# Kernel optimization log

Measured on AMD Instinct MI355X. Metric: run time of the kernel, lower is better.

The kernel has to match this reference:

```python
import jax, jax.numpy as jnp
import numpy as np
import math

N_EMB = 768
N_HEAD = 12
N_INNER = 3072
B, T = 2, 2048
EPS = 1e-4


def _gelu_tanh(x):
    return x * 0.5 * (1.0 + jnp.tanh(math.sqrt(2.0 / math.pi) * (x + 0.044715 * x ** 3)))


def _layernorm(x, scale, bias):
    mean = jnp.mean(x, axis=-1, keepdims=True)
    var = jnp.var(x, axis=-1, keepdims=True, ddof=1)  # torch.var default: unbiased
    return scale * ((x - mean) / jnp.sqrt(var + EPS)) + bias


def setup_inputs() -> dict:
    key = jax.random.key(0)
    ks = jax.random.split(key, 16)
    s_attn = 1.0 / math.sqrt(N_EMB)
    s_mlp1 = 1.0 / math.sqrt(N_EMB)
    s_mlp2 = 1.0 / math.sqrt(N_INNER)
    return {
        "x": jax.random.normal(ks[0], (B, T, N_EMB), dtype=jnp.float32),
        "Wq": jax.random.normal(ks[1], (N_EMB, N_EMB), dtype=jnp.float32) * s_attn,
        "bq": jnp.zeros((N_EMB,), jnp.float32),
        "Wk": jax.random.normal(ks[2], (N_EMB, N_EMB), dtype=jnp.float32) * s_attn,
        "bk": jnp.zeros((N_EMB,), jnp.float32),
        "Wv": jax.random.normal(ks[3], (N_EMB, N_EMB), dtype=jnp.float32) * s_attn,
        "bv": jnp.zeros((N_EMB,), jnp.float32),
        "Wo": jax.random.normal(ks[4], (N_EMB, N_EMB), dtype=jnp.float32) * s_attn,
        "bo": jnp.zeros((N_EMB,), jnp.float32),
        "ln1_s": jnp.ones((N_EMB,), jnp.float32),
        "ln1_b": jnp.zeros((N_EMB,), jnp.float32),
        "W1": jax.random.normal(ks[5], (N_EMB, N_INNER), dtype=jnp.float32) * s_mlp1,
        "b1": jnp.zeros((N_INNER,), jnp.float32),
        "W2": jax.random.normal(ks[6], (N_INNER, N_EMB), dtype=jnp.float32) * s_mlp2,
        "b2": jnp.zeros((N_EMB,), jnp.float32),
        "ln2_s": jnp.ones((N_EMB,), jnp.float32),
        "ln2_b": jnp.zeros((N_EMB,), jnp.float32),
    }


def reference(x, Wq, bq, Wk, bk, Wv, bv, Wo, bo, ln1_s, ln1_b, W1, b1, W2, b2, ln2_s, ln2_b):
    Bx, Tx, C = x.shape
    dh = C // N_HEAD
    # QKV projections -> [B, H, T, dh]
    def split_heads(y):
        return y.reshape(Bx, Tx, N_HEAD, dh).transpose(0, 2, 1, 3)
    q = split_heads(x @ Wq + bq)
    k = split_heads(x @ Wk + bk)
    v = split_heads(x @ Wv + bv)
    # naive full-score causal attention (materializes [B,H,T,T])
    scores = jnp.einsum("bhqd,bhkd->bhqk", q, k)
    causal = jnp.tril(jnp.ones((Tx, Tx), dtype=bool))
    scores = jnp.where(causal, scores, -jnp.inf)
    attn = jax.nn.softmax(scores / math.sqrt(dh), axis=-1)
    ctx = jnp.einsum("bhqk,bhkd->bhqd", attn, v)
    ctx = ctx.transpose(0, 2, 1, 3).reshape(Bx, Tx, C)
    attn_out = ctx @ Wo + bo
    # post-norm residual
    h = _layernorm(x + attn_out, ln1_s, ln1_b)
    mlp_out = _gelu_tanh(h @ W1 + b1) @ W2 + b2
    return _layernorm(h + mlp_out, ln2_s, ln2_b)
```

## Files before the change

kernel.cpp:

```cpp
#include <hip/hip_runtime.h>
#include <math.h>

#define TB  2
#define TT  2048
#define TC  768
#define TH  12
#define TDH 64
#define TI  3072
#define TM  (TB*TT)

typedef __attribute__((ext_vector_type(8))) __bf16 bf16x8;
typedef __attribute__((ext_vector_type(4))) __bf16 bf16x4;
typedef __attribute__((ext_vector_type(4))) float  f32x4;

__device__ __forceinline__ float gelu_tanh(float x) {
    float x3 = x * x * x;
    return 0.5f * x * (1.0f + tanhf(0.7978845608028654f * (x + 0.044715f * x3)));
}

__device__ __forceinline__ void gld_lds16(const void* g, void* l) {
    __builtin_amdgcn_global_load_lds(
        (const __attribute__((address_space(1))) unsigned int*)g,
        (__attribute__((address_space(3))) unsigned int*)l,
        16, 0, 0);
}

template<int N>
__device__ __forceinline__ void vmcnt_wait() {
    if constexpr (N == 0)      asm volatile("s_waitcnt vmcnt(0)" ::: "memory");
    else if constexpr (N == 2) asm volatile("s_waitcnt vmcnt(2)" ::: "memory");
    else if constexpr (N == 3) asm volatile("s_waitcnt vmcnt(3)" ::: "memory");
    else if constexpr (N == 4) asm volatile("s_waitcnt vmcnt(4)" ::: "memory");
    else if constexpr (N == 6) asm volatile("s_waitcnt vmcnt(6)" ::: "memory");
    else if constexpr (N == 8) asm volatile("s_waitcnt vmcnt(8)" ::: "memory");
    else static_assert(N == 0, "unsupported vmcnt");
}

#define BK 32

template<int BM_, int BN_, int WM_, int WN_, int THREADS_>
__global__ __launch_bounds__(THREADS_)
void gemm_mfma(const __bf16* __restrict__ A, const __bf16* __restrict__ Bt,
               const float* __restrict__ b0, const float* __restrict__ b1,
               const float* __restrict__ b2, const float* __restrict__ resid,
               float* __restrict__ outf, __bf16* __restrict__ outb,
               int N, int K, size_t wt_stride, size_t out_stride, int ep)
{
    constexpr int WAVES_N = BN_ / WN_;
    constexpr int TMt = WM_ / 16, TNt = WN_ / 16;
    constexpr int RP   = THREADS_ / 4;
    constexpr int AISS = BM_ / RP, BISS = BN_ / RP;
    constexpr int S    = AISS + BISS;
    constexpr int PASS = THREADS_ * 16;
    constexpr int TILE = (BM_ + BN_) * BK;
    static_assert(AISS >= 1 && BISS >= 1, "tile too small for thread count");
    __shared__ __align__(16) __bf16 lds[3 * TILE];

    const int tid  = threadIdx.x;
    const int wave = tid >> 6, lane = tid & 63;
    const int wm = wave / WAVES_N, wn = wave % WAVES_N;
    const int m0 = blockIdx.y * BM_, n0 = blockIdx.x * BN_;
    const int z  = blockIdx.z;

    const __bf16* Bz = Bt + (size_t)z * wt_stride;
    const size_t Kb = (size_t)K * 2;
    const char* Ag = (const char*)A + (size_t)m0 * Kb;
    const char* Bg = (const char*)Bz + (size_t)n0 * Kb;
    const int srow = tid >> 2;
    const int scol = ((tid & 3) ^ ((tid >> 4) & 3)) * 16;
    const int wbase = wave * 1024;

    f32x4 acc[TMt][TNt];
    #pragma unroll
    for (int i = 0; i < TMt; ++i)
        #pragma unroll
        for (int j = 0; j < TNt; ++j)
            acc[i][j] = (f32x4){0.f, 0.f, 0.f, 0.f};

    const int arow = wm * WM_ + (lane & 15);
    const int brow = wn * WN_ + (lane & 15);
    const int koff = (((lane >> 4) ^ ((lane >> 2) & 3))) * 8;

    const int nIter = K / BK;

    auto stage = [&](char* base, int k0b) {
        #pragma unroll
        for (int s = 0; s < AISS; ++s)
            gld_lds16(Ag + (size_t)(srow + RP * s) * Kb + k0b + scol,
                      base + s * PASS + wbase);
        char* bbase = base + BM_ * BK * 2;
        #pragma unroll
        for (int s = 0; s < BISS; ++s)
            gld_lds16(Bg + (size_t)(srow + RP * s) * Kb + k0b + scol,
                      bbase + s * PASS + wbase);
    };

    char* P0 = (char*)lds;
    char* P1 = P0 + (size_t)TILE * 2;
    char* P2 = P1 + (size_t)TILE * 2;

    stage(P0, 0);
    if (nIter > 1) stage(P1, BK * 2);
    __builtin_amdgcn_sched_barrier(0);
    char* cur = P0; char* n1 = P1; char* n2 = P2;

    for (int it = 0; it < nIter; ++it) {
        if (it + 2 < nIter) stage(n2, (it + 2) * (BK * 2));
        __builtin_amdgcn_sched_barrier(0);
        const int rem = nIter - 1 - it;
        if (rem >= 2)      vmcnt_wait<2 * S>();
        else if (rem == 1) vmcnt_wait<S>();
        else               vmcnt_wait<0>();
        __builtin_amdgcn_s_barrier();
        __builtin_amdgcn_sched_barrier(0);

        const __bf16* As = (const __bf16*)cur;
        const __bf16* Bs = As + BM_ * BK;
        bf16x8 af[TMt], bfr[TNt];
        #pragma unroll
        for (int ti = 0; ti < TMt; ++ti)
            af[ti] = *(const bf16x8*)&As[(arow + ti * 16) * BK + koff];
        #pragma unroll
        for (int tj = 0; tj < TNt; ++tj)
            bfr[tj] = *(const bf16x8*)&Bs[(brow + tj * 16) * BK + koff];
        #pragma unroll
        for (int ti = 0; ti < TMt; ++ti)
            #pragma unroll
            for (int tj = 0; tj < TNt; ++tj)
                acc[ti][tj] = __builtin_amdgcn_mfma_f32_16x16x32_bf16(
                    af[ti], bfr[tj], acc[ti][tj], 0, 0, 0);

        __builtin_amdgcn_sched_barrier(0);
        __builtin_amdgcn_s_barrier();
        char* t = cur; cur = n1; n1 = n2; n2 = t;
    }

    const int lrow = m0 + wm * WM_ + ((lane >> 4) << 2);
    const int lcol = n0 + wn * WN_ + (lane & 15);

    if (ep == 0) {
        const float* bias = (z == 0) ? b0 : (z == 1) ? b1 : b2;
        __bf16* outz = outb + (size_t)z * out_stride;
        if (z < 2) {
            #pragma unroll
            for (int tj = 0; tj < TNt; ++tj) {
                int n = lcol + tj * 16;
                float bj = bias[n];
                int h = n >> 6, d = n & 63;
                #pragma unroll
                for (int ti = 0; ti < TMt; ++ti)
                    #pragma unroll
                    for (int r = 0; r < 4; ++r) {
                        int m = lrow + ti * 16 + r;
                        int b = m >> 11, t = m & (TT - 1);
                        outz[((size_t)(b * TH + h) * TT + t) * TDH + d] =
                            (__bf16)(acc[ti][tj][r] + bj);
                    }
            }
        } else {
            #pragma unroll
            for (int tj = 0; tj < TNt; ++tj) {
                int n = lcol + tj * 16;
                float bj = bias[n];
                int h = n >> 6, d = n & 63;
                #pragma unroll
                for (int ti = 0; ti < TMt; ++ti) {
                    int m = lrow + ti * 16;
                    int b = m >> 11, t0 = m & (TT - 1);
                    bf16x4 pk;
                    #pragma unroll
                    for (int r = 0; r < 4; ++r)
                        pk[r] = (__bf16)(acc[ti][tj][r] + bj);
                    *(bf16x4*)(outz + ((size_t)(b * TH + h) * TDH + d) * TT + t0) = pk;
                }
            }
        }
    } else if (ep == 1) {
        #pragma unroll
        for (int tj = 0; tj < TNt; ++tj) {
            int n = lcol + tj * 16;
            float bj = b0[n];
            #pragma unroll
            for (int ti = 0; ti < TMt; ++ti)
                #pragma unroll
                for (int r = 0; r < 4; ++r) {
                    int m = lrow + ti * 16 + r;
                    outf[(size_t)m * N + n] =
                        acc[ti][tj][r] + bj + resid[(size_t)m * N + n];
                }
        }
    } else {
        #pragma unroll
        for (int tj = 0; tj < TNt; ++tj) {
            int n = lcol + tj * 16;
            float bj = b0[n];
            #pragma unroll
            for (int ti = 0; ti < TMt; ++ti)
                #pragma unroll
                for (int r = 0; r < 4; ++r) {
                    int m = lrow + ti * 16 + r;
                    outb[(size_t)m * N + n] = (__bf16)gelu_tanh(acc[ti][tj][r] + bj);
                }
        }
    }
}

__global__ __launch_bounds__(256)
void prep_kernel(const float* __restrict__ x,
                 const float* __restrict__ Wq, const float* __restrict__ Wk,
                 const float* __restrict__ Wv, const float* __restrict__ Wo,
                 const float* __restrict__ W1, const float* __restrict__ W2,
                 __bf16* __restrict__ x_bf, __bf16* __restrict__ WqkvT,
                 __bf16* __restrict__ WoT, __bf16* __restrict__ W1T,
                 __bf16* __restrict__ W2T)
{
    const size_t WSZ = (size_t)TC * TC;
    int bid = blockIdx.x;
    if (bid < 1536) {
        int i = (bid * 256 + threadIdx.x) * 8;
        float4 a = *(const float4*)(x + i);
        float4 b = *(const float4*)(x + i + 4);
        bf16x8 v;
        v[0] = (__bf16)a.x; v[1] = (__bf16)a.y; v[2] = (__bf16)a.z; v[3] = (__bf16)a.w;
        v[4] = (__bf16)b.x; v[5] = (__bf16)b.y; v[6] = (__bf16)b.z; v[7] = (__bf16)b.w;
        *(bf16x8*)(x_bf + i) = v;
        return;
    }
    bid -= 1536;
    const float* src; __bf16* dst; int K, N, tloc;
    if (bid < 2304) {
        int w = bid / 576; tloc = bid - w * 576;
        K = TC; N = TC;
        src = (w == 0) ? Wq : (w == 1) ? Wk : (w == 2) ? Wv : Wo;
        dst = (w < 3) ? (WqkvT + (size_t)w * WSZ) : WoT;
    } else if (bid < 4608) {
        tloc = bid - 2304; K = TC; N = TI; src = W1; dst = W1T;
    } else {
        tloc = bid - 4608; K = TI; N = TC; src = W2; dst = W2T;
    }
    int tiles_x = N >> 5;
    int n0 = (tloc % tiles_x) * 32, k0 = (tloc / tiles_x) * 32;

    __shared__ float tile[32][33];
    const int tx = threadIdx.x & 31, ty = threadIdx.x >> 5;
    #pragma unroll
    for (int i = 0; i < 32; i += 8)
        tile[ty + i][tx] = src[(size_t)(k0 + ty + i) * N + n0 + tx];
    __syncthreads();
    #pragma unroll
    for (int i = 0; i < 32; i += 8)
        dst[(size_t)(n0 + ty + i) * K + k0 + tx] = (__bf16)tile[tx][ty + i];
}

__global__ __launch_bounds__(256)
void ln_kernel(const float* __restrict__ in, const float* __restrict__ gs,
               const float* __restrict__ gb, float* __restrict__ out,
               __bf16* __restrict__ out_bf)
{
    const int row = blockIdx.x, tid = threadIdx.x;
    const float* r = in + (size_t)row * TC;
    float x0 = r[tid], x1 = r[tid + 256], x2 = r[tid + 512];
    float s = x0 + x1 + x2;
    float q = x0 * x0 + x1 * x1 + x2 * x2;
    #pragma unroll
    for (int off = 32; off > 0; off >>= 1) {
        s += __shfl_down(s, off);
        q += __shfl_down(q, off);
    }
    __shared__ float partial[8];
    __shared__ float stats[2];
    int wid = tid >> 6, lane = tid & 63;
    if (lane == 0) { partial[wid] = s; partial[wid + 4] = q; }
    __syncthreads();
    if (tid == 0) {
        float S = partial[0] + partial[1] + partial[2] + partial[3];
        float Q = partial[4] + partial[5] + partial[6] + partial[7];
        float mean = S * (1.0f / (float)TC);
        float var = (Q - (float)TC * mean * mean) * (1.0f / (float)(TC - 1));
        stats[0] = mean;
        stats[1] = rsqrtf(var + 1e-4f);
    }
    __syncthreads();
    float mean = stats[0], rstd = stats[1];
    float* w = out + (size_t)row * TC;
    float y0 = gs[tid]       * ((x0 - mean) * rstd) + gb[tid];
    float y1 = gs[tid + 256] * ((x1 - mean) * rstd) + gb[tid + 256];
    float y2 = gs[tid + 512] * ((x2 - mean) * rstd) + gb[tid + 512];
    w[tid] = y0; w[tid + 256] = y1; w[tid + 512] = y2;
    if (out_bf) {
        __bf16* wb = out_bf + (size_t)row * TC;
        wb[tid] = (__bf16)y0; wb[tid + 256] = (__bf16)y1; wb[tid + 512] = (__bf16)y2;
    }
}

#define AP 72
#define VP 136
#define ATT_SCALE 0.18033688011112042f

__global__ __launch_bounds__(256)
void attn_mfma(const __bf16* __restrict__ Q, const __bf16* __restrict__ K,
               const __bf16* __restrict__ Vt, __bf16* __restrict__ ctx)
{
    __shared__ __align__(16) __bf16 Ks[128 * AP];
    __shared__ __align__(16) __bf16 Vs[64 * VP];
    __shared__ __align__(16) __bf16 Ps[64 * VP];

    const int tid  = threadIdx.x;
    const int wave = tid >> 6, lane = tid & 63;
    const int c = lane & 15, g = lane >> 4;
    const int bh = blockIdx.y;
    const int qi = blockIdx.x;
    const int qt = (qi & 1) ? (31 - (qi >> 1)) : (qi >> 1);
    const int q_glob = qt * 64 + wave * 16 + c;

    const __bf16* Qb = Q  + (size_t)bh * TT * TDH;
    const __bf16* Kb = K  + (size_t)bh * TT * TDH;
    const __bf16* Vb = Vt + (size_t)bh * TDH * TT;

    bf16x8 qf0 = *(const bf16x8*)(Qb + (size_t)q_glob * TDH + g * 8);
    bf16x8 qf1 = *(const bf16x8*)(Qb + (size_t)q_glob * TDH + 32 + g * 8);

    const int krow = tid >> 3, kcol = (tid & 7) * 8;
    const int vrow = tid >> 4, vcol = (tid & 15) * 8;

    float m_i = -1e30f, l_i = 0.0f;
    f32x4 acc[4];
    #pragma unroll
    for (int m2 = 0; m2 < 4; ++m2) acc[m2] = (f32x4){0.f, 0.f, 0.f, 0.f};

    const int pmax = qt >> 1;
    for (int p = 0; p <= pmax; ++p) {
        const int kb = p * 128;
        bf16x8 kv[4], vv[4];
        #pragma unroll
        for (int s = 0; s < 4; ++s) {
            kv[s] = *(const bf16x8*)(Kb + (size_t)(kb + krow + 32 * s) * TDH + kcol);
            vv[s] = *(const bf16x8*)(Vb + (size_t)(vrow + 16 * s) * TT + kb + vcol);
        }
        __syncthreads();
        #pragma unroll
        for (int s = 0; s < 4; ++s) {
            *(bf16x8*)&Ks[(krow + 32 * s) * AP + kcol] = kv[s];
            *(bf16x8*)&Vs[(vrow + 16 * s) * VP + vcol] = vv[s];
        }
        __syncthreads();

        f32x4 st[8];
        #pragma unroll
        for (int g2 = 0; g2 < 8; ++g2) {
            bf16x8 af0 = *(const bf16x8*)&Ks[(16 * g2 + c) * AP + g * 8];
            bf16x8 af1 = *(const bf16x8*)&Ks[(16 * g2 + c) * AP + 32 + g * 8];
            f32x4 z = (f32x4){0.f, 0.f, 0.f, 0.f};
            z = __builtin_amdgcn_mfma_f32_16x16x32_bf16(af0, qf0, z, 0, 0, 0);
            z = __builtin_amdgcn_mfma_f32_16x16x32_bf16(af1, qf1, z, 0, 0, 0);
            st[g2] = z;
        }

        float sv[8][4];
        float mx = -1e30f;
        if (p == pmax) {
            #pragma unroll
            for (int g2 = 0; g2 < 8; ++g2)
                #pragma unroll
                for (int r = 0; r < 4; ++r) {
                    int kcol2 = kb + 16 * g2 + 4 * g + r;
                    float v = (kcol2 > q_glob) ? -1e30f : st[g2][r] * ATT_SCALE;
                    sv[g2][r] = v;
                    mx = fmaxf(mx, v);
                }
        } else {
            #pragma unroll
            for (int g2 = 0; g2 < 8; ++g2)
                #pragma unroll
                for (int r = 0; r < 4; ++r) {
                    float v = st[g2][r] * ATT_SCALE;
                    sv[g2][r] = v;
                    mx = fmaxf(mx, v);
                }
        }
        mx = fmaxf(mx, __shfl_xor(mx, 16));
        mx = fmaxf(mx, __shfl_xor(mx, 32));

        float nm = m_i;
        if (!__all(mx <= m_i + 8.0f)) {
            nm = fmaxf(m_i, mx);
            float corr = exp2f(m_i - nm);
            l_i *= corr;
            #pragma unroll
            for (int m2 = 0; m2 < 4; ++m2) {
                acc[m2][0] *= corr; acc[m2][1] *= corr;
                acc[m2][2] *= corr; acc[m2][3] *= corr;
            }
            m_i = nm;
        }

        float ps = 0.f;
        #pragma unroll
        for (int g2 = 0; g2 < 8; ++g2) {
            bf16x4 pk;
            #pragma unroll
            for (int r = 0; r < 4; ++r) {
                float pp = exp2f(sv[g2][r] - nm);
                ps += pp;
                pk[r] = (__bf16)pp;
            }
            *(bf16x4*)&Ps[(wave * 16 + c) * VP + 16 * g2 + 4 * g] = pk;
        }
        ps += __shfl_xor(ps, 16);
        ps += __shfl_xor(ps, 32);
        l_i += ps;

        bf16x8 pf[4];
        #pragma unroll
        for (int s = 0; s < 4; ++s)
            pf[s] = *(const bf16x8*)&Ps[(wave * 16 + c) * VP + 32 * s + g * 8];
        #pragma unroll
        for (int m2 = 0; m2 < 4; ++m2) {
            #pragma unroll
            for (int s = 0; s < 4; ++s) {
                bf16x8 vf = *(const bf16x8*)&Vs[(16 * m2 + c) * VP + 32 * s + g * 8];
                acc[m2] = __builtin_amdgcn_mfma_f32_16x16x32_bf16(vf, pf[s], acc[m2], 0, 0, 0);
            }
        }
    }

    const int b = bh / TH, h = bh - b * TH;
    float inv = 1.0f / l_i;
    #pragma unroll
    for (int m2 = 0; m2 < 4; ++m2) {
        bf16x4 o;
        #pragma unroll
        for (int r = 0; r < 4; ++r)
            o[r] = (__bf16)(acc[m2][r] * inv);
        *(bf16x4*)(ctx + ((size_t)b * TT + q_glob) * TC + h * TDH + 16 * m2 + 4 * g) = o;
    }
}

extern "C" void kernel_launch(void* const* d_in, const int* in_sizes, int n_in,
                              void* d_out, int out_size, void* d_ws, size_t ws_size,
                              hipStream_t stream)
{
    const float* x    = (const float*)d_in[0];
    const float* Wq   = (const float*)d_in[1];
    const float* bq   = (const float*)d_in[2];
    const float* Wk   = (const float*)d_in[3];
    const float* bk   = (const float*)d_in[4];
    const float* Wv   = (const float*)d_in[5];
    const float* bv   = (const float*)d_in[6];
    const float* Wo   = (const float*)d_in[7];
    const float* bo   = (const float*)d_in[8];
    const float* ln1s = (const float*)d_in[9];
    const float* ln1b = (const float*)d_in[10];
    const float* W1   = (const float*)d_in[11];
    const float* b1   = (const float*)d_in[12];
    const float* W2   = (const float*)d_in[13];
    const float* b2   = (const float*)d_in[14];
    const float* ln2s = (const float*)d_in[15];
    const float* ln2b = (const float*)d_in[16];
    float* out = (float*)d_out;

    const size_t MC  = (size_t)TM * TC;
    const size_t MCB = MC * 2;
    const size_t WSZ = (size_t)TC * TC;
    const size_t W12 = (size_t)TC * TI;

    char* W = (char*)d_ws;
    __bf16* qkvb  = (__bf16*)W;
    __bf16* x_bf  = (__bf16*)(W + 3 * MCB);
    float*  tmp1  = (float*)W;
    __bf16* u_bf  = (__bf16*)W;
    float*  h_f32 = (float*)(W + 4 * MCB);
    __bf16* ctxh  = (__bf16*)(W + 6 * MCB);
    __bf16* wts   = (__bf16*)(W + 7 * MCB);
    __bf16* WqkvT = wts;
    __bf16* WoT   = WqkvT + 3 * WSZ;
    __bf16* W1T   = WoT + WSZ;
    __bf16* W2T   = W1T + W12;

    prep_kernel<<<dim3(1536 + 6912), dim3(256), 0, stream>>>(
        x, Wq, Wk, Wv, Wo, W1, W2, x_bf, WqkvT, WoT, W1T, W2T);

    gemm_mfma<128, 128, 64, 32, 512><<<dim3(TC / 128, TM / 128, 3), dim3(512), 0, stream>>>(
        x_bf, WqkvT, bq, bk, bv, nullptr, nullptr, qkvb, TC, TC, WSZ, MC, 0);

    attn_mfma<<<dim3(TT / 64, TB * TH), dim3(256), 0, stream>>>(
        qkvb, qkvb + MC, qkvb + 2 * MC, ctxh);

    gemm_mfma<64, 64, 32, 32, 256><<<dim3(TC / 64, TM / 64, 1), dim3(256), 0, stream>>>(
        ctxh, WoT, bo, nullptr, nullptr, x, tmp1, nullptr, TC, TC, 0, 0, 1);

    ln_kernel<<<dim3(TM), dim3(256), 0, stream>>>(tmp1, ln1s, ln1b, h_f32, ctxh);

    gemm_mfma<128, 128, 64, 32, 512><<<dim3(TI / 128, TM / 128, 1), dim3(512), 0, stream>>>(
        ctxh, W1T, b1, nullptr, nullptr, nullptr, nullptr, u_bf, TI, TC, 0, 0, 2);

    gemm_mfma<64, 64, 32, 32, 256><<<dim3(TC / 64, TM / 64, 1), dim3(256), 0, stream>>>(
        u_bf, W2T, b2, nullptr, nullptr, h_f32, out, nullptr, TC, TI, 0, 0, 1);

    ln_kernel<<<dim3(TM), dim3(256), 0, stream>>>(out, ln2s, ln2b, out, nullptr);
}
```

Measured before the change: 312.0 us.

## Restructure attention to 32x32 MFMA with split-KV waves and swizzled LDS

The attention kernel now uses 32x32x16 bf16 MFMA instead of 16x16x32. Each pair of waves shares 32 query rows and the two pairs split each 128-key block into two 64-key halves, then merge their softmax states through LDS at the end. The K and V shared tiles drop their padding and use an XOR swizzle to avoid bank conflicts, and each wave gets a private P buffer. The aim is fewer LDS fragment reads and fewer shuffle reductions per tile, in exchange for an extra merge pass and higher register pressure from the 16-wide accumulators.

```diff
diff --git a/kernel.cpp b/kernel.cpp
--- a/kernel.cpp
+++ b/kernel.cpp
@@ -9,9 +9,10 @@
 #define TI  3072
 #define TM  (TB*TT)
 
-typedef __attribute__((ext_vector_type(8))) __bf16 bf16x8;
-typedef __attribute__((ext_vector_type(4))) __bf16 bf16x4;
-typedef __attribute__((ext_vector_type(4))) float  f32x4;
+typedef __attribute__((ext_vector_type(8)))  __bf16 bf16x8;
+typedef __attribute__((ext_vector_type(4)))  __bf16 bf16x4;
+typedef __attribute__((ext_vector_type(4)))  float  f32x4;
+typedef __attribute__((ext_vector_type(16))) float  f32x16;
 
 __device__ __forceinline__ float gelu_tanh(float x) {
     float x3 = x * x * x;
@@ -293,40 +294,48 @@
     }
 }
 
-#define AP 72
-#define VP 136
+#define PP 72
 #define ATT_SCALE 0.18033688011112042f
 
 __global__ __launch_bounds__(256)
 void attn_mfma(const __bf16* __restrict__ Q, const __bf16* __restrict__ K,
                const __bf16* __restrict__ Vt, __bf16* __restrict__ ctx)
 {
-    __shared__ __align__(16) __bf16 Ks[128 * AP];
-    __shared__ __align__(16) __bf16 Vs[64 * VP];
-    __shared__ __align__(16) __bf16 Ps[64 * VP];
+    __shared__ __align__(16) __bf16 Ks[128 * 64];
+    __shared__ __align__(16) __bf16 Vs[64 * 128];
+    __shared__ __align__(16) __bf16 Ps[4 * 32 * PP];
 
     const int tid  = threadIdx.x;
     const int wave = tid >> 6, lane = tid & 63;
-    const int c = lane & 15, g = lane >> 4;
+    const int l31 = lane & 31, h5 = lane >> 5, l7 = lane & 7;
+    const int q32  = wave & 1;
+    const int wgrp = wave >> 1;
     const int bh = blockIdx.y;
     const int qi = blockIdx.x;
     const int qt = (qi & 1) ? (31 - (qi >> 1)) : (qi >> 1);
-    const int q_glob = qt * 64 + wave * 16 + c;
+    const int q_glob = qt * 64 + q32 * 32 + l31;
 
     const __bf16* Qb = Q  + (size_t)bh * TT * TDH;
     const __bf16* Kb = K  + (size_t)bh * TT * TDH;
     const __bf16* Vb = Vt + (size_t)bh * TDH * TT;
 
-    bf16x8 qf0 = *(const bf16x8*)(Qb + (size_t)q_glob * TDH + g * 8);
-    bf16x8 qf1 = *(const bf16x8*)(Qb + (size_t)q_glob * TDH + 32 + g * 8);
-
-    const int krow = tid >> 3, kcol = (tid & 7) * 8;
-    const int vrow = tid >> 4, vcol = (tid & 15) * 8;
+    bf16x8 qf[4];
+    #pragma unroll
+    for (int ks = 0; ks < 4; ++ks)
+        qf[ks] = *(const bf16x8*)(Qb + (size_t)q_glob * TDH + ks * 16 + h5 * 8);
+
+    const int krow = tid >> 3;
+    const int kchW = ((tid & 7) ^ (krow & 7)) * 8;
+    const int vrow = tid >> 4;
+    const int vch  = tid & 15;
+    const int vchW = (((vch & 7) ^ (vrow & 7)) | (vch & 8)) * 8;
 
     float m_i = -1e30f, l_i = 0.0f;
-    f32x4 acc[4];
-    #pragma unroll
-    for (int m2 = 0; m2 < 4; ++m2) acc[m2] = (f32x4){0.f, 0.f, 0.f, 0.f};
+    f32x16 acc[2];
+    acc[0] = (f32x16)(0.0f);
+    acc[1] = (f32x16)(0.0f);
+
+    __bf16* PsW = Ps + wave * 32 * PP;
 
     const int pmax = qt >> 1;
     for (int p = 0; p <= pmax; ++p) {
@@ -334,105 +343,135 @@
         bf16x8 kv[4], vv[4];
         #pragma unroll
         for (int s = 0; s < 4; ++s) {
-            kv[s] = *(const bf16x8*)(Kb + (size_t)(kb + krow + 32 * s) * TDH + kcol);
-            vv[s] = *(const bf16x8*)(Vb + (size_t)(vrow + 16 * s) * TT + kb + vcol);
+            kv[s] = *(const bf16x8*)(Kb + (size_t)(kb + krow + 32 * s) * TDH + (tid & 7) * 8);
+            vv[s] = *(const bf16x8*)(Vb + (size_t)(vrow + 16 * s) * TT + kb + vch * 8);
         }
         __syncthreads();
         #pragma unroll
         for (int s = 0; s < 4; ++s) {
-            *(bf16x8*)&Ks[(krow + 32 * s) * AP + kcol] = kv[s];
-            *(bf16x8*)&Vs[(vrow + 16 * s) * VP + vcol] = vv[s];
+            *(bf16x8*)&Ks[(krow + 32 * s) * 64 + kchW]  = kv[s];
+            *(bf16x8*)&Vs[(vrow + 16 * s) * 128 + vchW] = vv[s];
         }
         __syncthreads();
 
-        f32x4 st[8];
-        #pragma unroll
-        for (int g2 = 0; g2 < 8; ++g2) {
-            bf16x8 af0 = *(const bf16x8*)&Ks[(16 * g2 + c) * AP + g * 8];
-            bf16x8 af1 = *(const bf16x8*)&Ks[(16 * g2 + c) * AP + 32 + g * 8];
-            f32x4 z = (f32x4){0.f, 0.f, 0.f, 0.f};
-            z = __builtin_amdgcn_mfma_f32_16x16x32_bf16(af0, qf0, z, 0, 0, 0);
-            z = __builtin_amdgcn_mfma_f32_16x16x32_bf16(af1, qf1, z, 0, 0, 0);
-            st[g2] = z;
-        }
-
-        float sv[8][4];
+        f32x16 st[2];
+        #pragma unroll
+        for (int t = 0; t < 2; ++t) {
+            const int rowk = wgrp * 64 + 32 * t + l31;
+            f32x16 z = (f32x16)(0.0f);
+            #pragma unroll
+            for (int ks = 0; ks < 4; ++ks) {
+                const int ch = ((ks * 2 + h5) ^ (l7)) * 8;
+                bf16x8 af = *(const bf16x8*)&Ks[rowk * 64 + ch];
+                z = __builtin_amdgcn_mfma_f32_32x32x16_bf16(af, qf[ks], z, 0, 0, 0);
+            }
+            st[t] = z;
+        }
+
         float mx = -1e30f;
         if (p == pmax) {
             #pragma unroll
-            for (int g2 = 0; g2 < 8; ++g2)
-                #pragma unroll
-                for (int r = 0; r < 4; ++r) {
-                    int kcol2 = kb + 16 * g2 + 4 * g + r;
-                    float v = (kcol2 > q_glob) ? -1e30f : st[g2][r] * ATT_SCALE;
-                    sv[g2][r] = v;
+            for (int t = 0; t < 2; ++t)
+                #pragma unroll
+                for (int r = 0; r < 16; ++r) {
+                    int kvg = kb + wgrp * 64 + 32 * t + (r & 3) + 8 * (r >> 2) + 4 * h5;
+                    float v = (kvg > q_glob) ? -1e30f : st[t][r] * ATT_SCALE;
+                    st[t][r] = v;
                     mx = fmaxf(mx, v);
                 }
         } else {
             #pragma unroll
-            for (int g2 = 0; g2 < 8; ++g2)
-                #pragma unroll
-                for (int r = 0; r < 4; ++r) {
-                    float v = st[g2][r] * ATT_SCALE;
-                    sv[g2][r] = v;
+            for (int t = 0; t < 2; ++t)
+                #pragma unroll
+                for (int r = 0; r < 16; ++r) {
+                    float v = st[t][r] * ATT_SCALE;
+                    st[t][r] = v;
                     mx = fmaxf(mx, v);
                 }
         }
-        mx = fmaxf(mx, __shfl_xor(mx, 16));
         mx = fmaxf(mx, __shfl_xor(mx, 32));
 
-        float nm = m_i;
         if (!__all(mx <= m_i + 8.0f)) {
-            nm = fmaxf(m_i, mx);
+            float nm = fmaxf(m_i, mx);
             float corr = exp2f(m_i - nm);
             l_i *= corr;
-            #pragma unroll
-            for (int m2 = 0; m2 < 4; ++m2) {
-                acc[m2][0] *= corr; acc[m2][1] *= corr;
-                acc[m2][2] *= corr; acc[m2][3] *= corr;
+            acc[0] *= corr;
+            acc[1] *= corr;
+            m_i = nm;
+        }
+
+        float ps = 0.f;
+        #pragma unroll
+        for (int t = 0; t < 2; ++t)
+            #pragma unroll
+            for (int a = 0; a < 4; ++a) {
+                bf16x4 pk;
+                #pragma unroll
+                for (int i = 0; i < 4; ++i) {
+                    float pp = exp2f(st[t][4 * a + i] - m_i);
+                    ps += pp;
+                    pk[i] = (__bf16)pp;
+                }
+                *(bf16x4*)&PsW[l31 * PP + 32 * t + 8 * a + 4 * h5] = pk;
             }
-            m_i = nm;
-        }
-
-        float ps = 0.f;
-        #pragma unroll
-        for (int g2 = 0; g2 < 8; ++g2) {
-            bf16x4 pk;
-            #pragma unroll
-            for (int r = 0; r < 4; ++r) {
-                float pp = exp2f(sv[g2][r] - nm);
-                ps += pp;
-                pk[r] = (__bf16)pp;
-            }
-            *(bf16x4*)&Ps[(wave * 16 + c) * VP + 16 * g2 + 4 * g] = pk;
-        }
-        ps += __shfl_xor(ps, 16);
         ps += __shfl_xor(ps, 32);
         l_i += ps;
 
         bf16x8 pf[4];
         #pragma unroll
-        for (int s = 0; s < 4; ++s)
-            pf[s] = *(const bf16x8*)&Ps[(wave * 16 + c) * VP + 32 * s + g * 8];
-        #pragma unroll
-        for (int m2 = 0; m2 < 4; ++m2) {
-            #pragma unroll
-            for (int s = 0; s < 4; ++s) {
-                bf16x8 vf = *(const bf16x8*)&Vs[(16 * m2 + c) * VP + 32 * s + g * 8];
-                acc[m2] = __builtin_amdgcn_mfma_f32_16x16x32_bf16(vf, pf[s], acc[m2], 0, 0, 0);
+        for (int ks = 0; ks < 4; ++ks)
+            pf[ks] = *(const bf16x8*)&PsW[l31 * PP + ks * 16 + h5 * 8];
+        #pragma unroll
+        for (int m2 = 0; m2 < 2; ++m2) {
+            const int d = m2 * 32 + l31;
+            #pragma unroll
+            for (int ks = 0; ks < 4; ++ks) {
+                const int ch = (wgrp * 8 + (((ks * 2 + h5) ^ (l7)))) * 8;
+                bf16x8 vf = *(const bf16x8*)&Vs[d * 128 + ch];
+                acc[m2] = __builtin_amdgcn_mfma_f32_32x32x16_bf16(vf, pf[ks], acc[m2], 0, 0, 0);
             }
         }
     }
 
-    const int b = bh / TH, h = bh - b * TH;
-    float inv = 1.0f / l_i;
-    #pragma unroll
-    for (int m2 = 0; m2 < 4; ++m2) {
-        bf16x4 o;
-        #pragma unroll
-        for (int r = 0; r < 4; ++r)
-            o[r] = (__bf16)(acc[m2][r] * inv);
-        *(bf16x4*)(ctx + ((size_t)b * TT + q_glob) * TC + h * TDH + 16 * m2 + 4 * g) = o;
+    __syncthreads();
+    float* accb0 = (float*)Ks;
+    float* accb1 = (float*)Ps;
+    float* mlb   = (float*)Vs;
+    if (wave >= 2) {
+        float* ab = (wave == 2) ? accb0 : accb1;
+        #pragma unroll
+        for (int m2 = 0; m2 < 2; ++m2)
+            #pragma unroll
+            for (int j = 0; j < 16; ++j)
+                ab[lane * 33 + m2 * 16 + j] = acc[m2][j];
+        mlb[(wave - 2) * 128 + lane] = m_i;
+        mlb[(wave - 2) * 128 + 64 + lane] = l_i;
+    }
+    __syncthreads();
+    if (wave < 2) {
+        float* ab = (wave == 0) ? accb0 : accb1;
+        float mo = mlb[wave * 128 + lane];
+        float lo = mlb[wave * 128 + 64 + lane];
+        float nm = fmaxf(m_i, mo);
+        float a = exp2f(m_i - nm), bw = exp2f(mo - nm);
+        float l = a * l_i + bw * lo;
+        float inv = 1.0f / l;
+        const int b = bh / TH, h = bh - b * TH;
+        #pragma unroll
+        for (int m2 = 0; m2 < 2; ++m2) {
+            #pragma unroll
+            for (int ag = 0; ag < 4; ++ag) {
+                bf16x4 o;
+                #pragma unroll
+                for (int i = 0; i < 4; ++i) {
+                    int r = 4 * ag + i;
+                    float v = a * acc[m2][r] + bw * ab[lane * 33 + m2 * 16 + r];
+                    o[i] = (__bf16)(v * inv);
+                }
+                int d0 = m2 * 32 + 8 * ag + 4 * h5;
+                *(bf16x4*)(ctx + ((size_t)b * TT + q_glob) * TC + h * TDH + d0) = o;
+            }
+        }
     }
 }
 
```

Measured after the change: 323.5 us. +3.7%, slower.

## Split-K the W2 GEMM with atomic accumulation onto LN1 output plus bias

Applied to the files above, without the earlier changes.

The down-projection GEMM (K=3072) is split into two K halves along grid z. Each half atomically adds its partial sums into the output buffer. The LN1 kernel pre-initialises that buffer with h + b2, which removes the separate residual read and the h_f32 buffer. This doubles the block count to fill more CUs on a long-K GEMM with few output tiles, at the cost of fp32 atomics on every output element and a non-deterministic summation order.

```diff
diff --git a/kernel.cpp b/kernel.cpp
--- a/kernel.cpp
+++ b/kernel.cpp
@@ -44,7 +44,8 @@
                const float* __restrict__ b0, const float* __restrict__ b1,
                const float* __restrict__ b2, const float* __restrict__ resid,
                float* __restrict__ outf, __bf16* __restrict__ outb,
-               int N, int K, size_t wt_stride, size_t out_stride, int ep)
+               int N, int K, int Krow, size_t wt_stride, size_t a_zoff,
+               size_t out_stride, int ep)
 {
     constexpr int WAVES_N = BN_ / WN_;
     constexpr int TMt = WM_ / 16, TNt = WN_ / 16;
@@ -63,8 +64,8 @@
     const int z  = blockIdx.z;
 
     const __bf16* Bz = Bt + (size_t)z * wt_stride;
-    const size_t Kb = (size_t)K * 2;
-    const char* Ag = (const char*)A + (size_t)m0 * Kb;
+    const size_t Kb = (size_t)Krow * 2;
+    const char* Ag = (const char*)A + (size_t)m0 * Kb + (size_t)z * a_zoff;
     const char* Bg = (const char*)Bz + (size_t)n0 * Kb;
     const int srow = tid >> 2;
     const int scol = ((tid & 3) ^ ((tid >> 4) & 3)) * 16;
@@ -189,7 +190,7 @@
                         acc[ti][tj][r] + bj + resid[(size_t)m * N + n];
                 }
         }
-    } else {
+    } else if (ep == 2) {
         #pragma unroll
         for (int tj = 0; tj < TNt; ++tj) {
             int n = lcol + tj * 16;
@@ -200,6 +201,18 @@
                 for (int r = 0; r < 4; ++r) {
                     int m = lrow + ti * 16 + r;
                     outb[(size_t)m * N + n] = (__bf16)gelu_tanh(acc[ti][tj][r] + bj);
+                }
+        }
+    } else {
+        #pragma unroll
+        for (int tj = 0; tj < TNt; ++tj) {
+            int n = lcol + tj * 16;
+            #pragma unroll
+            for (int ti = 0; ti < TMt; ++ti)
+                #pragma unroll
+                for (int r = 0; r < 4; ++r) {
+                    int m = lrow + ti * 16 + r;
+                    atomicAdd(&outf[(size_t)m * N + n], acc[ti][tj][r]);
                 }
         }
     }
@@ -255,7 +268,8 @@
 __global__ __launch_bounds__(256)
 void ln_kernel(const float* __restrict__ in, const float* __restrict__ gs,
                const float* __restrict__ gb, float* __restrict__ out,
-               __bf16* __restrict__ out_bf)
+               __bf16* __restrict__ out_bf,
+               const float* __restrict__ ib, float* __restrict__ io)
 {
     const int row = blockIdx.x, tid = threadIdx.x;
     const float* r = in + (size_t)row * TC;
@@ -282,14 +296,22 @@
     }
     __syncthreads();
     float mean = stats[0], rstd = stats[1];
-    float* w = out + (size_t)row * TC;
     float y0 = gs[tid]       * ((x0 - mean) * rstd) + gb[tid];
     float y1 = gs[tid + 256] * ((x1 - mean) * rstd) + gb[tid + 256];
     float y2 = gs[tid + 512] * ((x2 - mean) * rstd) + gb[tid + 512];
-    w[tid] = y0; w[tid + 256] = y1; w[tid + 512] = y2;
+    if (out) {
+        float* w = out + (size_t)row * TC;
+        w[tid] = y0; w[tid + 256] = y1; w[tid + 512] = y2;
+    }
     if (out_bf) {
         __bf16* wb = out_bf + (size_t)row * TC;
         wb[tid] = (__bf16)y0; wb[tid + 256] = (__bf16)y1; wb[tid + 512] = (__bf16)y2;
+    }
+    if (io) {
+        float* w2 = io + (size_t)row * TC;
+        w2[tid]       = y0 + ib[tid];
+        w2[tid + 256] = y1 + ib[tid + 256];
+        w2[tid + 512] = y2 + ib[tid + 512];
     }
 }
 
@@ -469,7 +491,6 @@
     __bf16* x_bf  = (__bf16*)(W + 3 * MCB);
     float*  tmp1  = (float*)W;
     __bf16* u_bf  = (__bf16*)W;
-    float*  h_f32 = (float*)(W + 4 * MCB);
     __bf16* ctxh  = (__bf16*)(W + 6 * MCB);
     __bf16* wts   = (__bf16*)(W + 7 * MCB);
     __bf16* WqkvT = wts;
@@ -481,21 +502,24 @@
         x, Wq, Wk, Wv, Wo, W1, W2, x_bf, WqkvT, WoT, W1T, W2T);
 
     gemm_mfma<128, 128, 64, 32, 512><<<dim3(TC / 128, TM / 128, 3), dim3(512), 0, stream>>>(
-        x_bf, WqkvT, bq, bk, bv, nullptr, nullptr, qkvb, TC, TC, WSZ, MC, 0);
+        x_bf, WqkvT, bq, bk, bv, nullptr, nullptr, qkvb, TC, TC, TC, WSZ, 0, MC, 0);
 
     attn_mfma<<<dim3(TT / 64, TB * TH), dim3(256), 0, stream>>>(
         qkvb, qkvb + MC, qkvb + 2 * MC, ctxh);
 
     gemm_mfma<64, 64, 32, 32, 256><<<dim3(TC / 64, TM / 64, 1), dim3(256), 0, stream>>>(
-        ctxh, WoT, bo, nullptr, nullptr, x, tmp1, nullptr, TC, TC, 0, 0, 1);
-
-    ln_kernel<<<dim3(TM), dim3(256), 0, stream>>>(tmp1, ln1s, ln1b, h_f32, ctxh);
+        ctxh, WoT, bo, nullptr, nullptr, x, tmp1, nullptr, TC, TC, TC, 0, 0, 0, 1);
+
+    ln_kernel<<<dim3(TM), dim3(256), 0, stream>>>(
+        tmp1, ln1s, ln1b, nullptr, ctxh, b2, out);
 
     gemm_mfma<128, 128, 64, 32, 512><<<dim3(TI / 128, TM / 128, 1), dim3(512), 0, stream>>>(
-        ctxh, W1T, b1, nullptr, nullptr, nullptr, nullptr, u_bf, TI, TC, 0, 0, 2);
-
-    gemm_mfma<64, 64, 32, 32, 256><<<dim3(TC / 64, TM / 64, 1), dim3(256), 0, stream>>>(
-        u_bf, W2T, b2, nullptr, nullptr, h_f32, out, nullptr, TC, TI, 0, 0, 1);
-
-    ln_kernel<<<dim3(TM), dim3(256), 0, stream>>>(out, ln2s, ln2b, out, nullptr);
-}
+        ctxh, W1T, b1, nullptr, nullptr, nullptr, nullptr, u_bf, TI, TC, TC, 0, 0, 0, 2);
+
+    gemm_mfma<64, 64, 32, 32, 256><<<dim3(TC / 64, TM / 64, 2), dim3(256), 0, stream>>>(
+        u_bf, W2T, nullptr, nullptr, nullptr, nullptr, out, nullptr,
+        TC, TI / 2, TI, (size_t)(TI / 2), (size_t)TI, 0, 3);
+
+    ln_kernel<<<dim3(TM), dim3(256), 0, stream>>>(
+        out, ln2s, ln2b, out, nullptr, nullptr, nullptr);
+}
```

Result: no change. 315.6 us (+1.2%).
